# Kernel optimization log

Measured on AMD Instinct MI355X. Metric: run time of the kernel, lower is better.

The kernel has to match this reference:

```python
import jax, jax.numpy as jnp
import numpy as np

DIM = 256
HEADS = 8
HEAD_DIM = DIM // HEADS
B = 4
Wd, Hd = 48, 48
N = Wd * Hd  # 2304


def _layernorm(x, g, b, eps=1e-5):
    mu = jnp.mean(x, axis=-1, keepdims=True)
    var = jnp.mean(jnp.square(x - mu), axis=-1, keepdims=True)
    return (x - mu) * jax.lax.rsqrt(var + eps) * g + b


def _build_mask(mask):
    # Binarize: <1 -> 0, >0 -> 1 (identity on {0,1} inputs)
    m = (mask > 0).astype(jnp.float32)
    flat = m.reshape(B, m.shape[1], Hd * Wd)[:, 0, :]  # [B, N]
    # mask[b,i,j] zeroed where (flat[j]==0 & flat[i]==1) | (flat[j]==0 & flat[i]==0)
    col0 = flat[:, None, :] == 0   # varies along j
    row = flat[:, :, None]         # varies along i
    bad = (col0 & (row == 1)) | (col0 & (row == 0))
    return (~bad).astype(jnp.float32)  # [B, N, N]


def setup_inputs() -> dict:
    key = jax.random.key(0)
    ks = jax.random.split(key, 12)
    s = 0.02
    x = jax.random.normal(ks[0], (B, N, DIM), jnp.float32)
    mask = jax.random.randint(ks[1], (B, 1, Wd, Hd), 0, 2).astype(jnp.float32)
    inp = {
        "x": x,
        "mask": mask,
        "ln_g": jnp.ones((DIM,), jnp.float32),
        "ln_b": jnp.zeros((DIM,), jnp.float32),
        "Wq": jax.random.normal(ks[2], (DIM, DIM), jnp.float32) * s,
        "bq": jnp.zeros((DIM,), jnp.float32),
        "Wk": jax.random.normal(ks[3], (DIM, DIM), jnp.float32) * s,
        "bk": jnp.zeros((DIM,), jnp.float32),
        "Wv": jax.random.normal(ks[4], (DIM, DIM), jnp.float32) * s,
        "bv": jnp.zeros((DIM,), jnp.float32),
        "Wp": jax.random.normal(ks[5], (DIM, DIM), jnp.float32) * s,
        "bp": jnp.zeros((DIM,), jnp.float32),
    }
    return inp


def reference(x, mask, ln_g, ln_b, Wq, bq, Wk, bk, Wv, bv, Wp, bp):
    Bx, Nx, C = x.shape
    mask_f = _build_mask(mask)  # [B, N, N]
    xn = _layernorm(x, ln_g, ln_b)
    def heads(Wm, bm):
        return (xn @ Wm + bm).reshape(Bx, Nx, HEADS, HEAD_DIM).transpose(0, 2, 1, 3)
    q = heads(Wq, bq)
    k = heads(Wk, bk)
    v = heads(Wv, bv)
    # NOTE: no 1/sqrt(d) scaling in the original; multiplicative 0/1 mask pre-softmax
    attn = jnp.einsum("bhnd,bhmd->bhnm", q, k) * mask_f[:, None, :, :]
    attn = jax.nn.softmax(attn, axis=-1)
    out = jnp.einsum("bhnm,bhmd->bhnd", attn, v)
    out = out.transpose(0, 2, 1, 3).reshape(Bx, Nx, C)
    return out @ Wp + bp
```

## Files before the change

kernel.cpp:

```cpp
#include <hip/hip_runtime.h>
#include <math.h>

typedef __attribute__((ext_vector_type(8))) short short8;
typedef __attribute__((ext_vector_type(4))) float f32x4;

constexpr int B   = 4;
constexpr int N   = 2304;
constexpr int DIM = 256;
constexpr int NH  = 8;
constexpr int DH  = 32;
constexpr int M   = B * N;
constexpr int SLOTS = 2336;
constexpr int CST = SLOTS * DH;
constexpr int XPB = SLOTS * DIM;

__device__ inline unsigned short f2bf(float f) {
    union { float f; unsigned u; } c; c.f = f;
    unsigned u = c.u;
    u += 0x7fffu + ((u >> 16) & 1u);
    return (unsigned short)(u >> 16);
}
__device__ inline unsigned short f2bf_trunc(float f) {
    union { float f; unsigned u; } c; c.f = f;
    return (unsigned short)(c.u >> 16);
}
__device__ inline float bf2f(unsigned short h) {
    union { unsigned u; float f; } c; c.u = ((unsigned)h) << 16;
    return c.f;
}

__device__ inline size_t fo256(int r, int k) {
    return ((size_t)((r >> 4) * 8 + (k >> 5)) << 9)
         + (size_t)(((((k & 31) >> 3) << 4) + (r & 15)) * 8 + (k & 7));
}
__device__ inline size_t foQK(int n, int d) {
    return ((size_t)(n >> 4) << 9)
         + (size_t)((((d >> 3) << 4) + (n & 15)) * 8 + (d & 7));
}
__device__ inline size_t foVTC(int d, int key) {
    return ((size_t)((d >> 4) * (SLOTS / 32) + (key >> 5)) << 9)
         + (size_t)(((((key & 31) >> 3) << 4) + (d & 15)) * 8 + (key & 7));
}

__global__ __launch_bounds__(256) void prep_kernel(
    const float* __restrict__ x, const float* __restrict__ g,
    const float* __restrict__ bta, unsigned short* __restrict__ xh,
    const float* __restrict__ Wq, const float* __restrict__ Wk,
    const float* __restrict__ Wv, const float* __restrict__ Wp,
    unsigned short* __restrict__ Wth, unsigned short* __restrict__ Wtl,
    const float* __restrict__ mask, int* __restrict__ inv,
    int* __restrict__ ncp, float* __restrict__ vm)
{
    __shared__ float tbuf[32][33];
    __shared__ int wsum[4];
    int bx = blockIdx.x;
    int t = threadIdx.x;
    if (bx < 2304) {
        int wave = t >> 6, lane = t & 63;
        int row = bx * 4 + wave;
        float4 v = *(const float4*)&x[(size_t)row * DIM + lane * 4];
        float s = v.x + v.y + v.z + v.w;
        #pragma unroll
        for (int o = 32; o > 0; o >>= 1) s += __shfl_xor(s, o, 64);
        float mu = s * (1.0f / DIM);
        float d0 = v.x - mu, d1 = v.y - mu, d2 = v.z - mu, d3 = v.w - mu;
        float s2 = d0 * d0 + d1 * d1 + d2 * d2 + d3 * d3;
        #pragma unroll
        for (int o = 32; o > 0; o >>= 1) s2 += __shfl_xor(s2, o, 64);
        float r = rsqrtf(s2 * (1.0f / DIM) + 1e-5f);
        float4 gg = *(const float4*)&g[lane * 4];
        float4 bb = *(const float4*)&bta[lane * 4];
        ushort4 hi;
        hi.x = f2bf(d0 * r * gg.x + bb.x);
        hi.y = f2bf(d1 * r * gg.y + bb.y);
        hi.z = f2bf(d2 * r * gg.z + bb.z);
        hi.w = f2bf(d3 * r * gg.w + bb.w);
        *(ushort4*)&xh[fo256(row, lane * 4)] = hi;
    } else if (bx < 2560) {
        int idx = bx - 2304;
        int z = idx >> 6, w = idx & 63;
        const float* W = (z == 0) ? Wq : (z == 1) ? Wk : (z == 2) ? Wv : Wp;
        unsigned short* oh = Wth + (size_t)z * DIM * DIM;
        unsigned short* ol = Wtl + (size_t)z * DIM * DIM;
        int tx = t & 31, ty0 = t >> 5;
        int n0 = (w & 7) * 32, k0 = (w >> 3) * 32;
        for (int ty = ty0; ty < 32; ty += 8)
            tbuf[ty][tx] = W[(size_t)(k0 + ty) * DIM + n0 + tx];
        __syncthreads();
        for (int nn = ty0; nn < 32; nn += 8) {
            float v = tbuf[tx][nn];
            unsigned short hh = f2bf(v);
            size_t o = fo256(n0 + nn, k0 + tx);
            oh[o] = hh;
            ol[o] = f2bf(v - bf2f(hh));
        }
    } else {
        int b = bx - 2560;
        int wave = t >> 6, lane = t & 63;
        vm[b * 256 + t] = 0.f;
        int cnt = 0;
        for (int j = t; j < N; j += 256) cnt += (mask[(size_t)b * N + j] > 0.f);
        #pragma unroll
        for (int o = 32; o > 0; o >>= 1) cnt += __shfl_down(cnt, o, 64);
        if (lane == 0) wsum[wave] = cnt;
        __syncthreads();
        int Nc = wsum[0] + wsum[1] + wsum[2] + wsum[3];
        int Nkp = (Nc + 31) & ~31;
        if (t == 0) { ncp[b * 2] = Nc; ncp[b * 2 + 1] = Nkp; }
        int baseK = 0;
        for (int j0 = 0; j0 < N; j0 += 256) {
            int j = j0 + t;
            bool keep = mask[(size_t)b * N + j] > 0.f;
            unsigned long long bal = __ballot(keep);
            int pos = __popcll(bal & ((1ull << lane) - 1ull));
            int wc  = __popcll(bal);
            __syncthreads();
            if (lane == 0) wsum[wave] = wc;
            __syncthreads();
            int wb = 0;
            for (int w = 0; w < wave; ++w) wb += wsum[w];
            int tot = wsum[0] + wsum[1] + wsum[2] + wsum[3];
            int keptBefore = baseK + wb + pos;
            if (keep) inv[(size_t)b * SLOTS + keptBefore] = j;
            else      inv[(size_t)b * SLOTS + Nkp + (j - keptBefore)] = j;
            baseK += tot;
        }
    }
}

__global__ __launch_bounds__(256) void permute_x(
    const unsigned short* __restrict__ xh,
    const int* __restrict__ inv, const int* __restrict__ ncp,
    unsigned short* __restrict__ xph)
{
    int tid = threadIdx.x;
    int wave = tid >> 6, lane = tid & 63;
    int kq = lane >> 4, r = lane & 15;
    int rtg = blockIdx.x * 4 + wave;
    int b = rtg / (SLOTS / 16), rt = rtg % (SLOTS / 16);
    int y = blockIdx.y;
    unsigned short* dst = xph + (size_t)b * XPB;
    int slot = rt * 16 + r;
    int Nc = ncp[b * 2], Nkp = ncp[b * 2 + 1];
    int mend = Nkp + (N - Nc);
    bool pad = (slot >= Nc && slot < Nkp) || slot >= mend;
    int n = pad ? -1 : inv[(size_t)b * SLOTS + slot];
    #pragma unroll
    for (int kt = 0; kt < 4; ++kt) {
        int k0 = (y * 4 + kt) * 32;
        short8 v = {0, 0, 0, 0, 0, 0, 0, 0};
        if (n >= 0) {
            int gn = b * N + n;
            v = *(const short8*)&xh[(((size_t)(gn >> 4) * 8 + (k0 >> 5)) << 9)
                                    + (kq * 16 + (gn & 15)) * 8];
        }
        *(short8*)&dst[(((size_t)(rt * 8 + (k0 >> 5))) << 9) + lane * 8] = v;
    }
}

__global__ __launch_bounds__(256, 4) void gemm_qkv(
    const unsigned short* __restrict__ xh,
    const unsigned short* __restrict__ xph,
    const unsigned short* __restrict__ Wth,
    const float* __restrict__ bq, const float* __restrict__ bk,
    const float* __restrict__ bv, const int* __restrict__ ncp,
    unsigned short* __restrict__ qb, unsigned short* __restrict__ kc,
    unsigned short* __restrict__ vc)
{
    constexpr size_t WSZ = (size_t)DIM * DIM;
    int z = blockIdx.z, bx = blockIdx.x;
    int tid = threadIdx.x;
    int wave = tid >> 6, lane = tid & 63;
    int quad = lane >> 4, l16 = lane & 15;
    const unsigned short *PA, *PB;
    int arow0, brow0, b;
    if (z == 0) {
        if (bx >= 576) return;
        arow0 = (bx >> 3) * 128 + wave * 32;
        brow0 = (bx & 7) * 32;
        b = ((bx >> 3) * 128) / N;
        PA = xh; PB = Wth;
    } else if (z == 1) {
        b = bx / 152;
        int rr = bx % 152;
        arow0 = (rr >> 3) * 128 + wave * 32;
        brow0 = (rr & 7) * 32;
        if (arow0 >= SLOTS) return;
        if (arow0 >= ncp[b * 2 + 1]) return;
        PA = xph + (size_t)b * XPB;
        PB = Wth + WSZ;
    } else {
        if (bx >= 584) return;
        int nidx = bx % 292;
        b = nidx / 73;
        arow0 = (bx / 292) * 128 + wave * 32;
        brow0 = (nidx % 73) * 32;
        PA = Wth + 2 * WSZ;
        PB = xph + (size_t)b * XPB;
    }
    f32x4 acc[2][2] = {};
    #pragma unroll
    for (int k0 = 0; k0 < DIM; k0 += 32) {
        size_t at = (((size_t)(arow0 >> 4) * 8 + (k0 >> 5)) << 9) + lane * 8;
        size_t bt = (((size_t)(brow0 >> 4) * 8 + (k0 >> 5)) << 9) + lane * 8;
        short8 a0 = *(const short8*)&PA[at];
        short8 a1 = *(const short8*)&PA[at + 4096];
        short8 b0 = *(const short8*)&PB[bt];
        short8 b1 = *(const short8*)&PB[bt + 4096];
        acc[0][0] = __builtin_amdgcn_mfma_f32_16x16x32_bf16(a0, b0, acc[0][0], 0, 0, 0);
        acc[0][1] = __builtin_amdgcn_mfma_f32_16x16x32_bf16(a0, b1, acc[0][1], 0, 0, 0);
        acc[1][0] = __builtin_amdgcn_mfma_f32_16x16x32_bf16(a1, b0, acc[1][0], 0, 0, 0);
        acc[1][1] = __builtin_amdgcn_mfma_f32_16x16x32_bf16(a1, b1, acc[1][1], 0, 0, 0);
    }
    if (z == 0) {
        int nbase = arow0 - b * N;
        #pragma unroll
        for (int j = 0; j < 2; ++j) {
            int c = brow0 + j * 16 + l16;
            int h = c >> 5, d = c & 31;
            float bs = bq[c];
            unsigned short* ob = qb + (size_t)(b * NH + h) * ((size_t)N * DH);
            #pragma unroll
            for (int i = 0; i < 2; ++i)
            #pragma unroll
            for (int r = 0; r < 4; ++r) {
                int n = nbase + i * 16 + quad * 4 + r;
                ob[foQK(n, d)] = f2bf(acc[i][j][r] + bs);
            }
        }
    } else if (z == 1) {
        #pragma unroll
        for (int j = 0; j < 2; ++j) {
            int c = brow0 + j * 16 + l16;
            int h = c >> 5, d = c & 31;
            float bs = bk[c];
            unsigned short* ob = kc + (size_t)(b * NH + h) * CST;
            #pragma unroll
            for (int i = 0; i < 2; ++i)
            #pragma unroll
            for (int r = 0; r < 4; ++r) {
                int slot = arow0 + i * 16 + quad * 4 + r;
                ob[foQK(slot, d)] = f2bf(acc[i][j][r] + bs);
            }
        }
    } else {
        #pragma unroll
        for (int i = 0; i < 2; ++i)
        #pragma unroll
        for (int r = 0; r < 4; ++r) {
            int m = arow0 + i * 16 + quad * 4 + r;
            int h = m >> 5, d = m & 31;
            float bs = bv[m];
            unsigned short* ob = vc + (size_t)(b * NH + h) * CST;
            #pragma unroll
            for (int j = 0; j < 2; ++j) {
                int key = brow0 + j * 16 + l16;
                ob[foVTC(d, key)] = f2bf(acc[i][j][r] + bs);
            }
        }
    }
}

__global__ __launch_bounds__(256) void vmsum_kernel(
    const unsigned short* __restrict__ vc, const int* __restrict__ ncp,
    float* __restrict__ vm)
{
    int bh = blockIdx.x, b = bh >> 3;
    int tid = threadIdx.x;
    int wave = tid >> 6, lane = tid & 63;
    int kq = lane >> 4, l16 = lane & 15;
    int Nc = ncp[b * 2], Nkp = ncp[b * 2 + 1];
    int mend = Nkp + (N - Nc);
    int tbeg = Nkp >> 5, tend = (mend + 31) >> 5;
    int wgid = blockIdx.y * 4 + wave;
    const int WSTEP = 32;
    const unsigned short* vcb = vc + (size_t)bh * CST;
    #pragma unroll
    for (int dt = 0; dt < 2; ++dt) {
        float s = 0.f;
        for (int t = tbeg + wgid; t < tend; t += WSTEP) {
            short8 v = *(const short8*)&vcb[((size_t)(dt * (SLOTS / 32) + t) << 9) + lane * 8];
            int keyb = t * 32 + kq * 8;
            #pragma unroll
            for (int j = 0; j < 8; ++j)
                s += (keyb + j < mend) ? bf2f((unsigned short)v[j]) : 0.f;
        }
        s += __shfl_xor(s, 16, 64);
        s += __shfl_xor(s, 32, 64);
        if (lane < 16) atomicAdd(&vm[bh * 32 + dt * 16 + l16], s);
    }
}

__global__ __launch_bounds__(256, 4) void attn_kernel(
    const unsigned short* __restrict__ Qb,
    const unsigned short* __restrict__ Kc,
    const unsigned short* __restrict__ Vc,
    const int* __restrict__ ncp,
    float* __restrict__ po, float* __restrict__ pl)
{
    __shared__ unsigned short pbuf[8 * 16 * 40];
    int tid  = threadIdx.x;
    int wave = tid >> 6, lane = tid & 63;
    int quad = lane >> 4, l16 = lane & 15;
    int bh = blockIdx.y, b = bh >> 3;
    int sp = blockIdx.z;
    int q0 = (blockIdx.x * 4 + wave) * 32;

    const unsigned short* Qf = Qb + (size_t)bh * ((size_t)N * DH);
    const unsigned short* Kf = Kc + (size_t)bh * CST;
    const unsigned short* Vf = Vc + (size_t)bh * CST;

    int Nc  = ncp[b * 2];
    int Nkp = ncp[b * 2 + 1];
    int chunks = Nkp >> 5;
    int cbeg = sp ? (chunks >> 1) : 0;
    int cend = sp ? chunks : (chunks >> 1);
    int kbeg = cbeg << 5, kend = cend << 5;

    short8 qA0 = *(const short8*)&Qf[((size_t)(q0 >> 4) << 9) + lane * 8];
    short8 qA1 = *(const short8*)&Qf[((size_t)((q0 >> 4) + 1) << 9) + lane * 8];

    f32x4 o00 = {0,0,0,0}, o01 = {0,0,0,0}, o10 = {0,0,0,0}, o11 = {0,0,0,0};
    float l0[4] = {0,0,0,0}, l1[4] = {0,0,0,0};

    unsigned short* pb0 = &pbuf[(wave * 2 + 0) * 640];
    unsigned short* pb1 = &pbuf[(wave * 2 + 1) * 640];

    short8 kB0 = *(const short8*)&Kf[((size_t)(kbeg >> 4) << 9) + lane * 8];
    short8 kB1 = *(const short8*)&Kf[((size_t)((kbeg >> 4) + 1) << 9) + lane * 8];
    short8 vB0 = *(const short8*)&Vf[((size_t)(kbeg >> 5) << 9) + lane * 8];
    short8 vB1 = *(const short8*)&Vf[((size_t)((SLOTS / 32) + (kbeg >> 5)) << 9) + lane * 8];

    for (int k0 = kbeg; k0 < kend; k0 += 32) {
        int kn = (k0 + 32 < kend) ? k0 + 32 : kbeg;
        short8 nk0 = *(const short8*)&Kf[((size_t)(kn >> 4) << 9) + lane * 8];
        short8 nk1 = *(const short8*)&Kf[((size_t)((kn >> 4) + 1) << 9) + lane * 8];
        short8 nv0 = *(const short8*)&Vf[((size_t)(kn >> 5) << 9) + lane * 8];
        short8 nv1 = *(const short8*)&Vf[((size_t)((SLOTS / 32) + (kn >> 5)) << 9) + lane * 8];

        bool in0 = (k0 + l16) < Nc;
        bool in1 = (k0 + 16 + l16) < Nc;
        f32x4 z = {0,0,0,0};
        f32x4 s00 = __builtin_amdgcn_mfma_f32_16x16x32_bf16(qA0, kB0, z, 0, 0, 0);
        f32x4 s01 = __builtin_amdgcn_mfma_f32_16x16x32_bf16(qA0, kB1, z, 0, 0, 0);
        f32x4 s10 = __builtin_amdgcn_mfma_f32_16x16x32_bf16(qA1, kB0, z, 0, 0, 0);
        f32x4 s11 = __builtin_amdgcn_mfma_f32_16x16x32_bf16(qA1, kB1, z, 0, 0, 0);
        #pragma unroll
        for (int r = 0; r < 4; ++r) {
            int row = quad * 4 + r;
            float p00 = in0 ? __expf(s00[r]) : 0.f;
            float p01 = in1 ? __expf(s01[r]) : 0.f;
            float p10 = in0 ? __expf(s10[r]) : 0.f;
            float p11 = in1 ? __expf(s11[r]) : 0.f;
            l0[r] += p00 + p01;
            l1[r] += p10 + p11;
            pb0[row * 40 + l16]      = f2bf_trunc(p00);
            pb0[row * 40 + 16 + l16] = f2bf_trunc(p01);
            pb1[row * 40 + l16]      = f2bf_trunc(p10);
            pb1[row * 40 + 16 + l16] = f2bf_trunc(p11);
        }
        short8 pA0 = *(const short8*)&pb0[l16 * 40 + quad * 8];
        short8 pA1 = *(const short8*)&pb1[l16 * 40 + quad * 8];
        o00 = __builtin_amdgcn_mfma_f32_16x16x32_bf16(pA0, vB0, o00, 0, 0, 0);
        o01 = __builtin_amdgcn_mfma_f32_16x16x32_bf16(pA0, vB1, o01, 0, 0, 0);
        o10 = __builtin_amdgcn_mfma_f32_16x16x32_bf16(pA1, vB0, o10, 0, 0, 0);
        o11 = __builtin_amdgcn_mfma_f32_16x16x32_bf16(pA1, vB1, o11, 0, 0, 0);

        kB0 = nk0; kB1 = nk1; vB0 = nv0; vB1 = nv1;
    }
    #pragma unroll
    for (int r = 0; r < 4; ++r) {
        #pragma unroll
        for (int off = 1; off < 16; off <<= 1) {
            l0[r] += __shfl_xor(l0[r], off, 64);
            l1[r] += __shfl_xor(l1[r], off, 64);
        }
    }
    size_t pbase = (size_t)(bh * 2 + sp) * N;
    #pragma unroll
    for (int r = 0; r < 4; ++r) {
        int row = quad * 4 + r;
        size_t b0 = (pbase + q0 + row) * DH;
        size_t b1 = (pbase + q0 + 16 + row) * DH;
        po[b0 + l16]      = o00[r];
        po[b0 + 16 + l16] = o01[r];
        po[b1 + l16]      = o10[r];
        po[b1 + 16 + l16] = o11[r];
        if (l16 == 0) {
            pl[pbase + q0 + row]      = l0[r];
            pl[pbase + q0 + 16 + row] = l1[r];
        }
    }
}

__global__ __launch_bounds__(256) void combine_kernel(
    const float* __restrict__ po, const float* __restrict__ pl,
    const float* __restrict__ vm, const int* __restrict__ ncp,
    unsigned short* __restrict__ ahn_hi, unsigned short* __restrict__ ahn_lo)
{
    int idx = blockIdx.x * 256 + threadIdx.x;
    int bhq = idx >> 2;
    int dg  = (idx & 3) * 8;
    int bh = bhq / N, q = bhq - bh * N;
    int b = bh >> 3, h = bh & 7;
    size_t p0 = ((size_t)(bh * 2 + 0) * N + q) * DH + dg;
    size_t p1 = ((size_t)(bh * 2 + 1) * N + q) * DH + dg;
    int Nc = ncp[b * 2];
    float l = pl[(size_t)(bh * 2) * N + q] + pl[(size_t)(bh * 2 + 1) * N + q]
            + (float)(N - Nc);
    float inv = 1.f / l;
    float4 a0 = *(const float4*)&po[p0];
    float4 a1 = *(const float4*)&po[p0 + 4];
    float4 c0 = *(const float4*)&po[p1];
    float4 c1 = *(const float4*)&po[p1 + 4];
    float4 m0 = *(const float4*)&vm[bh * 32 + dg];
    float4 m1 = *(const float4*)&vm[bh * 32 + dg + 4];
    float vals[8] = {
        (a0.x + c0.x + m0.x) * inv, (a0.y + c0.y + m0.y) * inv,
        (a0.z + c0.z + m0.z) * inv, (a0.w + c0.w + m0.w) * inv,
        (a1.x + c1.x + m1.x) * inv, (a1.y + c1.y + m1.y) * inv,
        (a1.z + c1.z + m1.z) * inv, (a1.w + c1.w + m1.w) * inv };
    union { unsigned short u[8]; short8 v; } hi, lo;
    #pragma unroll
    for (int j = 0; j < 8; ++j) {
        unsigned short t = f2bf(vals[j]);
        hi.u[j] = t;
        lo.u[j] = f2bf(vals[j] - bf2f(t));
    }
    size_t o = fo256(b * N + q, h * 32 + dg);
    *(short8*)&ahn_hi[o] = hi.v;
    *(short8*)&ahn_lo[o] = lo.v;
}

__global__ __launch_bounds__(256, 4) void gemm_p(
    const unsigned short* __restrict__ Ahi, const unsigned short* __restrict__ Alo,
    const unsigned short* __restrict__ Wth, const unsigned short* __restrict__ Wtl,
    const float* __restrict__ bias, float* __restrict__ out)
{
    constexpr size_t WSZ = (size_t)DIM * DIM;
    const unsigned short* Bhi = Wth + 3 * WSZ;
    const unsigned short* Blo = Wtl + 3 * WSZ;
    int tid = threadIdx.x;
    int wave = tid >> 6, lane = tid & 63;
    int quad = lane >> 4, l16 = lane & 15;
    int r0 = blockIdx.y * 128 + wave * 32;
    int c0 = blockIdx.x * 16;
    f32x4 acc0 = {}, acc1 = {};
    #pragma unroll
    for (int k0 = 0; k0 < DIM; k0 += 32) {
        size_t at = (((size_t)(r0 >> 4) * 8 + (k0 >> 5)) << 9) + lane * 8;
        size_t bt = (((size_t)(c0 >> 4) * 8 + (k0 >> 5)) << 9) + lane * 8;
        short8 ah0 = *(const short8*)&Ahi[at];
        short8 al0 = *(const short8*)&Alo[at];
        short8 ah1 = *(const short8*)&Ahi[at + 4096];
        short8 al1 = *(const short8*)&Alo[at + 4096];
        short8 bh = *(const short8*)&Bhi[bt];
        short8 bl = *(const short8*)&Blo[bt];
        acc0 = __builtin_amdgcn_mfma_f32_16x16x32_bf16(ah0, bh, acc0, 0, 0, 0);
        acc0 = __builtin_amdgcn_mfma_f32_16x16x32_bf16(ah0, bl, acc0, 0, 0, 0);
        acc0 = __builtin_amdgcn_mfma_f32_16x16x32_bf16(al0, bh, acc0, 0, 0, 0);
        acc1 = __builtin_amdgcn_mfma_f32_16x16x32_bf16(ah1, bh, acc1, 0, 0, 0);
        acc1 = __builtin_amdgcn_mfma_f32_16x16x32_bf16(ah1, bl, acc1, 0, 0, 0);
        acc1 = __builtin_amdgcn_mfma_f32_16x16x32_bf16(al1, bh, acc1, 0, 0, 0);
    }
    int c = c0 + l16;
    float bs = bias[c];
    #pragma unroll
    for (int r = 0; r < 4; ++r) {
        int R0 = r0 + quad * 4 + r;
        out[(size_t)R0 * DIM + c] = acc0[r] + bs;
        out[(size_t)(R0 + 16) * DIM + c] = acc1[r] + bs;
    }
}

extern "C" void kernel_launch(void* const* d_in, const int* in_sizes, int n_in,
                              void* d_out, int out_size, void* d_ws, size_t ws_size,
                              hipStream_t stream)
{
    const float* x    = (const float*)d_in[0];
    const float* mask = (const float*)d_in[1];
    const float* ln_g = (const float*)d_in[2];
    const float* ln_b = (const float*)d_in[3];
    const float* Wq   = (const float*)d_in[4];
    const float* bq   = (const float*)d_in[5];
    const float* Wk   = (const float*)d_in[6];
    const float* bk   = (const float*)d_in[7];
    const float* Wv   = (const float*)d_in[8];
    const float* bv   = (const float*)d_in[9];
    const float* Wp   = (const float*)d_in[10];
    const float* bp   = (const float*)d_in[11];
    float* out = (float*)d_out;

    constexpr size_t SZ  = (size_t)M * DIM;
    constexpr size_t CSZ = (size_t)B * NH * CST;
    constexpr size_t XSZ = (size_t)B * XPB;
    constexpr size_t WSZ = (size_t)DIM * DIM;
    unsigned short* p = (unsigned short*)d_ws;
    unsigned short* xh = p;  p += SZ;
    unsigned short* xph = p; p += XSZ;
    unsigned short* qb = p;  p += SZ;
    unsigned short* kc = p;  p += CSZ;
    unsigned short* vc = p;  p += CSZ;
    unsigned short* ah = p;  p += SZ;
    unsigned short* al = p;  p += SZ;
    unsigned short* wth = p; p += 4 * WSZ;
    unsigned short* wtl = p; p += 4 * WSZ;
    float* po = (float*)p;
    float* pl = po + (size_t)B * NH * 2 * N * DH;
    float* vm = pl + (size_t)B * NH * 2 * N;
    int* inv = (int*)(vm + (size_t)B * NH * 32);
    int* ncp = inv + (size_t)B * SLOTS;

    prep_kernel<<<2564, 256, 0, stream>>>(
        x, ln_g, ln_b, xh, Wq, Wk, Wv, Wp, wth, wtl, mask, inv, ncp, vm);

    permute_x<<<dim3((B * (SLOTS / 16)) / 4, 2), 256, 0, stream>>>(
        xh, inv, ncp, xph);

    gemm_qkv<<<dim3(608, 1, 3), 256, 0, stream>>>(
        xh, xph, wth, bq, bk, bv, ncp, qb, kc, vc);

    vmsum_kernel<<<dim3(B * NH, 8), 256, 0, stream>>>(vc, ncp, vm);

    attn_kernel<<<dim3(N / 128, B * NH, 2), 256, 0, stream>>>(
        qb, kc, vc, ncp, po, pl);

    combine_kernel<<<(B * NH * N * 4) / 256, 256, 0, stream>>>(
        po, pl, vm, ncp, ah, al);

    gemm_p<<<dim3(DIM / 16, M / 128), 256, 0, stream>>>(
        ah, al, wth, wtl, bp, out);
}
```

Baseline: 161.5 us.

## Fold vmsum into attention grid, interleave K layout for packed P stores, drop lo split

Removes the separate vmsum kernel launch by giving the attention launch a third z-slice whose first blocks compute the V column sums. It also reorders the K cache so that each lane holds adjacent key pairs, which lets the P tile be written to LDS as packed 32-bit stores instead of four 16-bit stores. Finally, the attention output's hi/lo bf16 split is dropped, so gemm_p does one fewer MFMA per tile and reads half as much A data. That last step gives up precision in the projection input. The vmsum slice also wastes many early-exit blocks and launches in the same kernel as the attention work.

```diff
diff --git a/kernel.cpp b/kernel.cpp
--- a/kernel.cpp
+++ b/kernel.cpp
@@ -20,14 +20,13 @@
     u += 0x7fffu + ((u >> 16) & 1u);
     return (unsigned short)(u >> 16);
 }
-__device__ inline unsigned short f2bf_trunc(float f) {
-    union { float f; unsigned u; } c; c.f = f;
-    return (unsigned short)(c.u >> 16);
-}
 __device__ inline float bf2f(unsigned short h) {
     union { unsigned u; float f; } c; c.u = ((unsigned)h) << 16;
     return c.f;
 }
+__device__ inline unsigned bits(float f) {
+    union { float f; unsigned u; } c; c.f = f; return c.u;
+}
 
 __device__ inline size_t fo256(int r, int k) {
     return ((size_t)((r >> 4) * 8 + (k >> 5)) << 9)
@@ -36,6 +35,12 @@
 __device__ inline size_t foQK(int n, int d) {
     return ((size_t)(n >> 4) << 9)
          + (size_t)((((d >> 3) << 4) + (n & 15)) * 8 + (d & 7));
+}
+__device__ inline size_t foKI(int slot, int d) {
+    int tile = ((slot >> 5) << 1) + (slot & 1);
+    int npos = (slot & 31) >> 1;
+    return ((size_t)tile << 9)
+         + (size_t)((((d >> 3) << 4) + npos) * 8 + (d & 7));
 }
 __device__ inline size_t foVTC(int d, int key) {
     return ((size_t)((d >> 4) * (SLOTS / 32) + (key >> 5)) << 9)
@@ -240,7 +245,7 @@
             #pragma unroll
             for (int r = 0; r < 4; ++r) {
                 int slot = arow0 + i * 16 + quad * 4 + r;
-                ob[foQK(slot, d)] = f2bf(acc[i][j][r] + bs);
+                ob[foKI(slot, d)] = f2bf(acc[i][j][r] + bs);
             }
         }
     } else {
@@ -261,42 +266,13 @@
     }
 }
 
-__global__ __launch_bounds__(256) void vmsum_kernel(
-    const unsigned short* __restrict__ vc, const int* __restrict__ ncp,
-    float* __restrict__ vm)
-{
-    int bh = blockIdx.x, b = bh >> 3;
-    int tid = threadIdx.x;
-    int wave = tid >> 6, lane = tid & 63;
-    int kq = lane >> 4, l16 = lane & 15;
-    int Nc = ncp[b * 2], Nkp = ncp[b * 2 + 1];
-    int mend = Nkp + (N - Nc);
-    int tbeg = Nkp >> 5, tend = (mend + 31) >> 5;
-    int wgid = blockIdx.y * 4 + wave;
-    const int WSTEP = 32;
-    const unsigned short* vcb = vc + (size_t)bh * CST;
-    #pragma unroll
-    for (int dt = 0; dt < 2; ++dt) {
-        float s = 0.f;
-        for (int t = tbeg + wgid; t < tend; t += WSTEP) {
-            short8 v = *(const short8*)&vcb[((size_t)(dt * (SLOTS / 32) + t) << 9) + lane * 8];
-            int keyb = t * 32 + kq * 8;
-            #pragma unroll
-            for (int j = 0; j < 8; ++j)
-                s += (keyb + j < mend) ? bf2f((unsigned short)v[j]) : 0.f;
-        }
-        s += __shfl_xor(s, 16, 64);
-        s += __shfl_xor(s, 32, 64);
-        if (lane < 16) atomicAdd(&vm[bh * 32 + dt * 16 + l16], s);
-    }
-}
-
 __global__ __launch_bounds__(256, 4) void attn_kernel(
     const unsigned short* __restrict__ Qb,
     const unsigned short* __restrict__ Kc,
     const unsigned short* __restrict__ Vc,
     const int* __restrict__ ncp,
-    float* __restrict__ po, float* __restrict__ pl)
+    float* __restrict__ po, float* __restrict__ pl,
+    float* __restrict__ vm)
 {
     __shared__ unsigned short pbuf[8 * 16 * 40];
     int tid  = threadIdx.x;
@@ -304,8 +280,33 @@
     int quad = lane >> 4, l16 = lane & 15;
     int bh = blockIdx.y, b = bh >> 3;
     int sp = blockIdx.z;
+
+    if (sp == 2) {
+        if (blockIdx.x >= 8) return;
+        int kq = quad;
+        int Nc = ncp[b * 2], Nkp = ncp[b * 2 + 1];
+        int mend = Nkp + (N - Nc);
+        int tbeg = Nkp >> 5, tend = (mend + 31) >> 5;
+        int wgid = blockIdx.x * 4 + wave;
+        const unsigned short* vcb = Vc + (size_t)bh * CST;
+        #pragma unroll
+        for (int dt = 0; dt < 2; ++dt) {
+            float s = 0.f;
+            for (int t = tbeg + wgid; t < tend; t += 32) {
+                short8 v = *(const short8*)&vcb[((size_t)(dt * (SLOTS / 32) + t) << 9) + lane * 8];
+                int keyb = t * 32 + kq * 8;
+                #pragma unroll
+                for (int j = 0; j < 8; ++j)
+                    s += (keyb + j < mend) ? bf2f((unsigned short)v[j]) : 0.f;
+            }
+            s += __shfl_xor(s, 16, 64);
+            s += __shfl_xor(s, 32, 64);
+            if (lane < 16) atomicAdd(&vm[bh * 32 + dt * 16 + l16], s);
+        }
+        return;
+    }
+
     int q0 = (blockIdx.x * 4 + wave) * 32;
-
     const unsigned short* Qf = Qb + (size_t)bh * ((size_t)N * DH);
     const unsigned short* Kf = Kc + (size_t)bh * CST;
     const unsigned short* Vf = Vc + (size_t)bh * CST;
@@ -338,8 +339,9 @@
         short8 nv0 = *(const short8*)&Vf[((size_t)(kn >> 5) << 9) + lane * 8];
         short8 nv1 = *(const short8*)&Vf[((size_t)((SLOTS / 32) + (kn >> 5)) << 9) + lane * 8];
 
-        bool in0 = (k0 + l16) < Nc;
-        bool in1 = (k0 + 16 + l16) < Nc;
+        int key0 = k0 + 2 * l16;
+        bool in0 = key0 < Nc;
+        bool in1 = key0 + 1 < Nc;
         f32x4 z = {0,0,0,0};
         f32x4 s00 = __builtin_amdgcn_mfma_f32_16x16x32_bf16(qA0, kB0, z, 0, 0, 0);
         f32x4 s01 = __builtin_amdgcn_mfma_f32_16x16x32_bf16(qA0, kB1, z, 0, 0, 0);
@@ -354,10 +356,10 @@
             float p11 = in1 ? __expf(s11[r]) : 0.f;
             l0[r] += p00 + p01;
             l1[r] += p10 + p11;
-            pb0[row * 40 + l16]      = f2bf_trunc(p00);
-            pb0[row * 40 + 16 + l16] = f2bf_trunc(p01);
-            pb1[row * 40 + l16]      = f2bf_trunc(p10);
-            pb1[row * 40 + 16 + l16] = f2bf_trunc(p11);
+            unsigned pk0 = (bits(p00) >> 16) | (bits(p01) & 0xffff0000u);
+            unsigned pk1 = (bits(p10) >> 16) | (bits(p11) & 0xffff0000u);
+            *(unsigned*)&pb0[row * 40 + 2 * l16] = pk0;
+            *(unsigned*)&pb1[row * 40 + 2 * l16] = pk1;
         }
         short8 pA0 = *(const short8*)&pb0[l16 * 40 + quad * 8];
         short8 pA1 = *(const short8*)&pb1[l16 * 40 + quad * 8];
@@ -396,7 +398,7 @@
 __global__ __launch_bounds__(256) void combine_kernel(
     const float* __restrict__ po, const float* __restrict__ pl,
     const float* __restrict__ vm, const int* __restrict__ ncp,
-    unsigned short* __restrict__ ahn_hi, unsigned short* __restrict__ ahn_lo)
+    unsigned short* __restrict__ ahn_hi)
 {
     int idx = blockIdx.x * 256 + threadIdx.x;
     int bhq = idx >> 2;
@@ -415,25 +417,20 @@
     float4 c1 = *(const float4*)&po[p1 + 4];
     float4 m0 = *(const float4*)&vm[bh * 32 + dg];
     float4 m1 = *(const float4*)&vm[bh * 32 + dg + 4];
-    float vals[8] = {
-        (a0.x + c0.x + m0.x) * inv, (a0.y + c0.y + m0.y) * inv,
-        (a0.z + c0.z + m0.z) * inv, (a0.w + c0.w + m0.w) * inv,
-        (a1.x + c1.x + m1.x) * inv, (a1.y + c1.y + m1.y) * inv,
-        (a1.z + c1.z + m1.z) * inv, (a1.w + c1.w + m1.w) * inv };
-    union { unsigned short u[8]; short8 v; } hi, lo;
-    #pragma unroll
-    for (int j = 0; j < 8; ++j) {
-        unsigned short t = f2bf(vals[j]);
-        hi.u[j] = t;
-        lo.u[j] = f2bf(vals[j] - bf2f(t));
-    }
-    size_t o = fo256(b * N + q, h * 32 + dg);
-    *(short8*)&ahn_hi[o] = hi.v;
-    *(short8*)&ahn_lo[o] = lo.v;
+    union { unsigned short u[8]; short8 v; } hi;
+    hi.u[0] = f2bf((a0.x + c0.x + m0.x) * inv);
+    hi.u[1] = f2bf((a0.y + c0.y + m0.y) * inv);
+    hi.u[2] = f2bf((a0.z + c0.z + m0.z) * inv);
+    hi.u[3] = f2bf((a0.w + c0.w + m0.w) * inv);
+    hi.u[4] = f2bf((a1.x + c1.x + m1.x) * inv);
+    hi.u[5] = f2bf((a1.y + c1.y + m1.y) * inv);
+    hi.u[6] = f2bf((a1.z + c1.z + m1.z) * inv);
+    hi.u[7] = f2bf((a1.w + c1.w + m1.w) * inv);
+    *(short8*)&ahn_hi[fo256(b * N + q, h * 32 + dg)] = hi.v;
 }
 
 __global__ __launch_bounds__(256, 4) void gemm_p(
-    const unsigned short* __restrict__ Ahi, const unsigned short* __restrict__ Alo,
+    const unsigned short* __restrict__ Ahi,
     const unsigned short* __restrict__ Wth, const unsigned short* __restrict__ Wtl,
     const float* __restrict__ bias, float* __restrict__ out)
 {
@@ -451,17 +448,13 @@
         size_t at = (((size_t)(r0 >> 4) * 8 + (k0 >> 5)) << 9) + lane * 8;
         size_t bt = (((size_t)(c0 >> 4) * 8 + (k0 >> 5)) << 9) + lane * 8;
         short8 ah0 = *(const short8*)&Ahi[at];
-        short8 al0 = *(const short8*)&Alo[at];
         short8 ah1 = *(const short8*)&Ahi[at + 4096];
-        short8 al1 = *(const short8*)&Alo[at + 4096];
         short8 bh = *(const short8*)&Bhi[bt];
         short8 bl = *(const short8*)&Blo[bt];
         acc0 = __builtin_amdgcn_mfma_f32_16x16x32_bf16(ah0, bh, acc0, 0, 0, 0);
         acc0 = __builtin_amdgcn_mfma_f32_16x16x32_bf16(ah0, bl, acc0, 0, 0, 0);
-        acc0 = __builtin_amdgcn_mfma_f32_16x16x32_bf16(al0, bh, acc0, 0, 0, 0);
         acc1 = __builtin_amdgcn_mfma_f32_16x16x32_bf16(ah1, bh, acc1, 0, 0, 0);
         acc1 = __builtin_amdgcn_mfma_f32_16x16x32_bf16(ah1, bl, acc1, 0, 0, 0);
-        acc1 = __builtin_amdgcn_mfma_f32_16x16x32_bf16(al1, bh, acc1, 0, 0, 0);
     }
     int c = c0 + l16;
     float bs = bias[c];
@@ -502,7 +495,6 @@
     unsigned short* kc = p;  p += CSZ;
     unsigned short* vc = p;  p += CSZ;
     unsigned short* ah = p;  p += SZ;
-    unsigned short* al = p;  p += SZ;
     unsigned short* wth = p; p += 4 * WSZ;
     unsigned short* wtl = p; p += 4 * WSZ;
     float* po = (float*)p;
@@ -520,14 +512,12 @@
     gemm_qkv<<<dim3(608, 1, 3), 256, 0, stream>>>(
         xh, xph, wth, bq, bk, bv, ncp, qb, kc, vc);
 
-    vmsum_kernel<<<dim3(B * NH, 8), 256, 0, stream>>>(vc, ncp, vm);
-
-    attn_kernel<<<dim3(N / 128, B * NH, 2), 256, 0, stream>>>(
-        qb, kc, vc, ncp, po, pl);
+    attn_kernel<<<dim3(N / 128, B * NH, 3), 256, 0, stream>>>(
+        qb, kc, vc, ncp, po, pl, vm);
 
     combine_kernel<<<(B * NH * N * 4) / 256, 256, 0, stream>>>(
-        po, pl, vm, ncp, ah, al);
+        po, pl, vm, ncp, ah);
 
     gemm_p<<<dim3(DIM / 16, M / 128), 256, 0, stream>>>(
-        ah, al, wth, wtl, bp, out);
-}
+        ah, wth, wtl, bp, out);
+}
```

Measured after the change: 150.7 us. 1.07x faster.
